# Kernel tuning notes

Measured on AMD Instinct MI355X. Metric: run time of the kernel, lower is better.

## Reference

```python
import jax, jax.numpy as jnp
import numpy as np
from jax import lax

RANK = 4
N_ITERS = 20  # fixed ALS iteration count (tensorly default caps at 100 with tol; fixed count for jit)
EPS = 1e-6


def _khatri_rao(U, V):
    # column-wise Kronecker: (m, r) x (n, r) -> (m*n, r), row index i*n + j
    r = U.shape[1]
    return (U[:, None, :] * V[None, :, :]).reshape(-1, r)


def _cp_als_mode0(T, A, B, C):
    # CP-ALS on 3-way tensor T [I,J,K]; returns mode-0 factor A [I, r]
    I, J, K = T.shape
    T0 = T.reshape(I, J * K)                       # cols indexed j*K+k
    T1 = jnp.moveaxis(T, 1, 0).reshape(J, I * K)   # cols indexed i*K+k
    T2 = jnp.moveaxis(T, 2, 0).reshape(K, I * J)   # cols indexed i*J+j
    eye = EPS * jnp.eye(RANK, dtype=T.dtype)

    def step(carry, _):
        A, B, C = carry
        G = (B.T @ B) * (C.T @ C) + eye
        A = jnp.linalg.solve(G, (T0 @ _khatri_rao(B, C)).T).T
        G = (A.T @ A) * (C.T @ C) + eye
        B = jnp.linalg.solve(G, (T1 @ _khatri_rao(A, C)).T).T
        G = (A.T @ A) * (B.T @ B) + eye
        C = jnp.linalg.solve(G, (T2 @ _khatri_rao(A, B)).T).T
        return (A, B, C), None

    (A, B, C), _ = lax.scan(step, (A, B, C), None, length=N_ITERS)
    return A


def setup_inputs() -> dict:
    key = jax.random.key(0)
    ks = jax.random.split(key, 8)
    b, c, h, w = 256, 512, 14, 14
    red = 16
    x = jax.random.uniform(ks[0], (b, c, h, w), dtype=jnp.float32)
    # random ALS init factors (per sample)
    A0 = jax.random.uniform(ks[1], (b, c, RANK), dtype=jnp.float32)
    B0 = jax.random.uniform(ks[2], (b, h, RANK), dtype=jnp.float32)
    C0 = jax.random.uniform(ks[3], (b, w, RANK), dtype=jnp.float32)
    # rank_fc: Linear(rank,rank,bias=False), Linear(rank,1,bias=False)
    w1 = jax.random.normal(ks[4], (RANK, RANK), dtype=jnp.float32) / np.sqrt(RANK)
    w2 = jax.random.normal(ks[5], (1, RANK), dtype=jnp.float32) / np.sqrt(RANK)
    # fc: Linear(c, c//red), Linear(c//red, c)
    fw1 = jax.random.normal(ks[6], (c // red, c), dtype=jnp.float32) / np.sqrt(c)
    fw2 = jax.random.normal(ks[7], (c, c // red), dtype=jnp.float32) / np.sqrt(c // red)
    return {"x": x, "A0": A0, "B0": B0, "C0": C0, "w1": w1, "w2": w2, "fw1": fw1, "fw2": fw2}


def reference(x, A0, B0, C0, w1, w2, fw1, fw2):
    b, c, _, _ = x.shape
    # per-sample CP decomposition; keep channel-mode factor [b, c, rank]
    A = jax.vmap(_cp_als_mode0)(x, A0, B0, C0)
    # rank_fc: (b,c,rank) -> (b,c)
    y = jnp.maximum(jnp.einsum('bcr,sr->bcs', A, w1), 0.0)
    y = jnp.einsum('bcs,os->bco', y, w2)[..., 0]
    # SE fc: (b,c) -> sigmoid gate
    y = jnp.maximum(y @ fw1.T, 0.0)
    y = jax.nn.sigmoid(y @ fw2.T)
    return x * y[:, :, None, None]
```

## Files before the change

kernel.cpp:

```cpp
#include <hip/hip_runtime.h>


#define EPSV 1e-6f

#define SM_ATA  104

typedef __attribute__((ext_vector_type(8))) short short8;
typedef __attribute__((ext_vector_type(4))) float float4v;

struct SMem {
  union {
    struct {
      short xhi[4 * 13 * 64 * 8];
      short xlo[4 * 13 * 64 * 8];
    } p1;
    struct {
      union {
        float gram[196 * 197];
        struct {
          short fh[7 * 64 * 8];
          short fl[7 * 64 * 8];
          float part[512 * 5];
        } f;
      } g;
      float H[196 * 5];
      float Y[196 * 5];
    } p2;
  } u;
  float B[56];
  float C[56];
  float Sm[120];
};

__device__ __forceinline__ float rlane(float v, int l) {
  return __uint_as_float(__builtin_amdgcn_readlane(__float_as_uint(v), l));
}
__device__ __forceinline__ void fence_lds() { __threadfence_block(); }

__device__ __forceinline__ unsigned bf16rne(float f) {
  unsigned u = __float_as_uint(f);
  return (u + 0x7FFFu + ((u >> 16) & 1u)) >> 16;
}

__device__ __forceinline__ float gram16(const float* V, int l) {
  int r = (l >> 2) & 3, s = l & 3;
  float a = 0.f;
#pragma unroll
  for (int j = 0; j < 14; ++j) a += V[j * 4 + r] * V[j * 4 + s];
  return a;
}

__device__ __forceinline__ float sel4(float a, float b, float c, float d, int k) {
  float x = (k & 1) ? b : a;
  float y = (k & 1) ? d : c;
  return (k & 2) ? y : x;
}

__device__ __forceinline__ void ginv_lanes(float myG, float gv[16]) {
  const float a00 = rlane(myG, 0),  a01 = rlane(myG, 1),  a02 = rlane(myG, 2),  a03 = rlane(myG, 3);
  const float a10 = rlane(myG, 4),  a11 = rlane(myG, 5),  a12 = rlane(myG, 6),  a13 = rlane(myG, 7);
  const float a20 = rlane(myG, 8),  a21 = rlane(myG, 9),  a22 = rlane(myG, 10), a23 = rlane(myG, 11);
  const float a30 = rlane(myG, 12), a31 = rlane(myG, 13), a32 = rlane(myG, 14), a33 = rlane(myG, 15);
  const float s0 = a00*a11 - a10*a01, s1 = a00*a12 - a10*a02, s2 = a00*a13 - a10*a03;
  const float s3 = a01*a12 - a11*a02, s4 = a01*a13 - a11*a03, s5 = a02*a13 - a12*a03;
  const float c5 = a22*a33 - a32*a23, c4 = a21*a33 - a31*a23, c3 = a21*a32 - a31*a22;
  const float c2 = a20*a33 - a30*a23, c1 = a20*a32 - a30*a22, c0 = a20*a31 - a30*a21;
  const float det = s0*c5 - s1*c4 + s2*c3 + s3*c2 - s4*c1 + s5*c0;
  const float rd = 1.0f / det;
  gv[0]  = ( a11*c5 - a12*c4 + a13*c3) * rd;
  gv[1]  = (-a01*c5 + a02*c4 - a03*c3) * rd;
  gv[2]  = ( a31*s5 - a32*s4 + a33*s3) * rd;
  gv[3]  = (-a21*s5 + a22*s4 - a23*s3) * rd;
  gv[4]  = (-a10*c5 + a12*c2 - a13*c1) * rd;
  gv[5]  = ( a00*c5 - a02*c2 + a03*c1) * rd;
  gv[6]  = (-a30*s5 + a32*s2 - a33*s1) * rd;
  gv[7]  = ( a20*s5 - a22*s2 + a23*s1) * rd;
  gv[8]  = ( a10*c4 - a11*c2 + a13*c0) * rd;
  gv[9]  = (-a00*c4 + a01*c2 - a03*c0) * rd;
  gv[10] = ( a30*s4 - a31*s2 + a33*s0) * rd;
  gv[11] = (-a20*s4 + a21*s2 - a23*s0) * rd;
  gv[12] = (-a10*c3 + a11*c1 - a12*c0) * rd;
  gv[13] = ( a00*c3 - a01*c1 + a02*c0) * rd;
  gv[14] = (-a30*s3 + a31*s1 - a32*s0) * rd;
  gv[15] = ( a20*s3 - a21*s1 + a22*s0) * rd;
}

__device__ __forceinline__ void computeH_scatter(SMem* sm, int l, const float gv[16]) {
#pragma unroll
  for (int k4 = 0; k4 < 4; ++k4) {
    int p = l + 64 * k4;
    if (p < 196) {
      int j = p / 14, kk = p - j * 14;
      float kr[4];
#pragma unroll
      for (int s = 0; s < 4; ++s) kr[s] = sm->B[j * 4 + s] * sm->C[kk * 4 + s];
      int kb = p >> 5, ii = p & 7, lrow = ((p >> 3) & 3) * 16;
#pragma unroll
      for (int r = 0; r < 4; ++r) {
        float h = kr[0] * gv[0 + r] + kr[1] * gv[4 + r]
                + kr[2] * gv[8 + r] + kr[3] * gv[12 + r];
        sm->u.p2.H[p * 5 + r] = h;
        unsigned hh = bf16rne(h);
        float hf = __uint_as_float(hh << 16);
        unsigned ll = bf16rne(h - hf);
        int fi = (kb * 64 + lrow + r) * 8 + ii;
        sm->u.p2.g.f.fh[fi] = (short)hh;
        sm->u.p2.g.f.fl[fi] = (short)ll;
      }
    }
  }
}

__device__ __forceinline__ void initial_H(SMem* sm, int l) {
  float btb = gram16(sm->B, l);
  float ctc = gram16(sm->C, l);
  float dgl = ((l >> 2) == (l & 3)) ? EPSV : 0.f;
  float myG = btb * ctc + dgl;
  float gv[16];
  ginv_lanes(myG, gv);
  computeH_scatter(sm, l, gv);
}

__device__ __forceinline__ void factor_update(SMem* sm, int l) {
  const int jj = l >> 2, r = l & 3;
  const float dgl = ((l >> 2) == (l & 3)) ? EPSV : 0.f;
  float gv[16];
  float btb_new;
  {
    float ctc_old = gram16(sm->C, l);
    float ata = sm->Sm[SM_ATA + (l & 15)];
    ginv_lanes(ata * ctc_old + dgl, gv);
    float m = 0.f;
    if (l < 56) {
#pragma unroll
      for (int k = 0; k < 14; ++k) m += sm->u.p2.Y[(jj * 14 + k) * 5 + r] * sm->C[k * 4 + r];
    }
    float bn = 0.f;
#pragma unroll
    for (int e = 0; e < 4; ++e) {
      float me = e ? __shfl_xor(m, e, 64) : m;
      float coef = sel4(gv[((0 ^ e) << 2) + 0], gv[((1 ^ e) << 2) + 1],
                        gv[((2 ^ e) << 2) + 2], gv[((3 ^ e) << 2) + 3], r);
      bn += me * coef;
    }
    if (l < 56) sm->B[l] = bn;
  }
  fence_lds();
  {
    btb_new = gram16(sm->B, l);
    float ata = sm->Sm[SM_ATA + (l & 15)];
    ginv_lanes(ata * btb_new + dgl, gv);
    float m = 0.f;
    if (l < 56) {
#pragma unroll
      for (int j = 0; j < 14; ++j) m += sm->u.p2.Y[(j * 14 + jj) * 5 + r] * sm->B[j * 4 + r];
    }
    float cn = 0.f;
#pragma unroll
    for (int e = 0; e < 4; ++e) {
      float me = e ? __shfl_xor(m, e, 64) : m;
      float coef = sel4(gv[((0 ^ e) << 2) + 0], gv[((1 ^ e) << 2) + 1],
                        gv[((2 ^ e) << 2) + 2], gv[((3 ^ e) << 2) + 3], r);
      cn += me * coef;
    }
    if (l < 56) sm->C[l] = cn;
  }
  fence_lds();
  {
    float ctc_new = gram16(sm->C, l);
    ginv_lanes(btb_new * ctc_new + dgl, gv);
    computeH_scatter(sm, l, gv);
  }
}

extern "C" __global__ void __launch_bounds__(1024, 4)
dese_kernel(const float* __restrict__ x, const float* __restrict__ B0,
            const float* __restrict__ C0, const float* __restrict__ w1,
            const float* __restrict__ w2, const float* __restrict__ fw1,
            const float* __restrict__ fw2, float* __restrict__ out) {
  extern __shared__ char smraw[];
  SMem* sm = (SMem*)smraw;
  const int tid = threadIdx.x;
  const int b = blockIdx.x;
  const int wv = tid >> 6;
  const int lane = tid & 63;
  const float* xb = x + (size_t)b * 100352;

  if (tid < 56) sm->B[tid] = B0[b * 56 + tid];
  if (tid >= 64 && tid < 120) sm->C[tid - 64] = C0[b * 56 + (tid - 64)];

  {
    const int R = (wv >= 4) + (wv >= 7) + (wv >= 10) + (wv >= 12) + (wv >= 14) + (wv >= 15);
    const int base = (R == 0) ? 0 : (R == 1) ? 4 : (R == 2) ? 7 : (R == 3) ? 10
                   : (R == 4) ? 12 : (R == 5) ? 14 : 15;
    const int I0 = 2 * R;
    const int J0 = I0 + 4 * (wv - base);
    const int IC1 = (I0 + 1 <= 12) ? I0 + 1 : 12;
    const bool iok1 = (I0 + 1 <= 12);

    float4v acc0[4], acc1[4];
#pragma unroll
    for (int i = 0; i < 4; ++i) {
      acc0[i] = (float4v){0.f, 0.f, 0.f, 0.f};
      acc1[i] = (float4v){0.f, 0.f, 0.f, 0.f};
    }

    for (int chunk = 0; chunk < 4; ++chunk) {
      __syncthreads();
#pragma unroll
      for (int t = 0; t < 4; ++t) {
        int u = wv + 16 * t;
        if (u < 52) {
          int s = u / 13, pt = u - s * 13;
          int p = pt * 16 + (lane & 15);
          int chb = chunk * 128 + s * 32 + (lane >> 4) * 8;
          unsigned hp[4], lp[4];
#pragma unroll
          for (int ii = 0; ii < 8; ++ii) {
            float v = 0.f;
            if (p < 196) v = xb[(size_t)(chb + ii) * 196 + p];
            unsigned h = bf16rne(v);
            float hf = __uint_as_float(h << 16);
            unsigned lo2 = bf16rne(v - hf);
            if (ii & 1) { hp[ii >> 1] |= (h << 16); lp[ii >> 1] |= (lo2 << 16); }
            else        { hp[ii >> 1] = h;          lp[ii >> 1] = lo2; }
          }
          int fidx = (s * 13 + pt) * 64 + lane;
          *(uint4*)&sm->u.p1.xhi[fidx * 8] = make_uint4(hp[0], hp[1], hp[2], hp[3]);
          *(uint4*)&sm->u.p1.xlo[fidx * 8] = make_uint4(lp[0], lp[1], lp[2], lp[3]);
        }
      }
      __syncthreads();
#pragma unroll
      for (int s = 0; s < 4; ++s) {
        const short8 aH0 = *(const short8*)&sm->u.p1.xhi[((s * 13 + I0)  * 64 + lane) * 8];
        const short8 aL0 = *(const short8*)&sm->u.p1.xlo[((s * 13 + I0)  * 64 + lane) * 8];
        const short8 aH1 = *(const short8*)&sm->u.p1.xhi[((s * 13 + IC1) * 64 + lane) * 8];
        const short8 aL1 = *(const short8*)&sm->u.p1.xlo[((s * 13 + IC1) * 64 + lane) * 8];
#pragma unroll
        for (int j = 0; j < 4; ++j) {
          const int J = J0 + j;
          if (J <= 12) {
            const short8 bH = *(const short8*)&sm->u.p1.xhi[((s * 13 + J) * 64 + lane) * 8];
            const short8 bL = *(const short8*)&sm->u.p1.xlo[((s * 13 + J) * 64 + lane) * 8];
            acc0[j] = __builtin_amdgcn_mfma_f32_16x16x32_bf16(aH0, bH, acc0[j], 0, 0, 0);
            acc0[j] = __builtin_amdgcn_mfma_f32_16x16x32_bf16(aH0, bL, acc0[j], 0, 0, 0);
            acc0[j] = __builtin_amdgcn_mfma_f32_16x16x32_bf16(aL0, bH, acc0[j], 0, 0, 0);
            if (iok1 && I0 + 1 <= J) {
              acc1[j] = __builtin_amdgcn_mfma_f32_16x16x32_bf16(aH1, bH, acc1[j], 0, 0, 0);
              acc1[j] = __builtin_amdgcn_mfma_f32_16x16x32_bf16(aH1, bL, acc1[j], 0, 0, 0);
              acc1[j] = __builtin_amdgcn_mfma_f32_16x16x32_bf16(aL1, bH, acc1[j], 0, 0, 0);
            }
          }
        }
      }
    }
    __syncthreads();
    {
      int col = lane & 15, quad = lane >> 4;
#define WRITE_TILE(ACC, I)                                          \
      {                                                             \
        int pc = (J0 + j) * 16 + col;                               \
        _Pragma("unroll")                                           \
        for (int reg = 0; reg < 4; ++reg) {                         \
          int pr = (I) * 16 + quad * 4 + reg;                       \
          if (pr < 196 && pc < 196) {                               \
            float v = ACC[j][reg];                                  \
            sm->u.p2.g.gram[pr * 197 + pc] = v;                     \
            sm->u.p2.g.gram[pc * 197 + pr] = v;                     \
          }                                                         \
        }                                                           \
      }
#pragma unroll
      for (int j = 0; j < 4; ++j) {
        const int J = J0 + j;
        if (J <= 12) {
          WRITE_TILE(acc0, I0)
          if (iok1 && I0 + 1 <= J) WRITE_TILE(acc1, I0 + 1)
        }
      }
#undef WRITE_TILE
    }
  }
  __syncthreads();

  short8 afh[7], afl[7];
  if (wv < 13) {
    const int m = wv * 16 + (lane & 15);
    const int mok = (m < 196);
    const int kq = (lane >> 4) * 8;
#pragma unroll
    for (int kb = 0; kb < 7; ++kb) {
#pragma unroll
      for (int i = 0; i < 8; ++i) {
        int k = kb * 32 + kq + i;
        float v = (mok && k < 196) ? sm->u.p2.g.gram[m * 197 + k] : 0.f;
        unsigned h = bf16rne(v);
        float hf = __uint_as_float(h << 16);
        unsigned lo = bf16rne(v - hf);
        afh[kb][i] = (short)h;
        afl[kb][i] = (short)lo;
      }
    }
  }
  __syncthreads();
  {
    unsigned* z = (unsigned*)sm->u.p2.g.f.fh;
#pragma unroll
    for (int t = 0; t < 4; ++t) {
      int idx = tid + 1024 * t;
      if (idx < 3584) z[idx] = 0u;
    }
  }
  __syncthreads();

  if (tid < 64) initial_H(sm, lane);
  __syncthreads();

  for (int it = 0; it < 19; ++it) {
    if (wv < 13) {
      float4v ac0 = {0.f, 0.f, 0.f, 0.f}, ac1 = {0.f, 0.f, 0.f, 0.f};
#pragma unroll
      for (int kb = 0; kb < 7; ++kb) {
        const short8 bh = *(const short8*)&sm->u.p2.g.f.fh[(kb * 64 + lane) * 8];
        const short8 bl = *(const short8*)&sm->u.p2.g.f.fl[(kb * 64 + lane) * 8];
        if (kb & 1) {
          ac1 = __builtin_amdgcn_mfma_f32_16x16x32_bf16(afh[kb], bh, ac1, 0, 0, 0);
          ac1 = __builtin_amdgcn_mfma_f32_16x16x32_bf16(afh[kb], bl, ac1, 0, 0, 0);
          ac1 = __builtin_amdgcn_mfma_f32_16x16x32_bf16(afl[kb], bh, ac1, 0, 0, 0);
        } else {
          ac0 = __builtin_amdgcn_mfma_f32_16x16x32_bf16(afh[kb], bh, ac0, 0, 0, 0);
          ac0 = __builtin_amdgcn_mfma_f32_16x16x32_bf16(afh[kb], bl, ac0, 0, 0, 0);
          ac0 = __builtin_amdgcn_mfma_f32_16x16x32_bf16(afl[kb], bh, ac0, 0, 0, 0);
        }
      }
      float4v acc = ac0 + ac1;
      int col = lane & 15;
      int row0 = wv * 16 + ((lane >> 4) << 2);
      if (col < 4) {
#pragma unroll
        for (int reg = 0; reg < 4; ++reg) {
          int pr = row0 + reg;
          if (pr < 196) sm->u.p2.Y[pr * 5 + col] = acc[reg];
        }
      }
    }
    __syncthreads();
    {
      int r = wv >> 2, s = wv & 3;
      float a = 0.f;
#pragma unroll
      for (int k4 = 0; k4 < 4; ++k4) {
        int p = lane + 64 * k4;
        if (p < 196) a += sm->u.p2.H[p * 5 + r] * sm->u.p2.Y[p * 5 + s];
      }
#pragma unroll
      for (int m = 32; m > 0; m >>= 1) a += __shfl_xor(a, m, 64);
      if (lane == 0) sm->Sm[SM_ATA + wv] = a;
    }
    __syncthreads();
    if (tid < 64) factor_update(sm, lane);
    __syncthreads();
  }

  {
    float hr[13];
#pragma unroll
    for (int k = 0; k < 13; ++k) {
      int d = 64 * k + lane;
      hr[k] = (d < 784) ? sm->u.p2.H[(d >> 2) * 5 + (d & 3)] : 0.f;
    }
    const int ch = tid & 511;
    const int half = tid >> 9;
    const float4* row = (const float4*)(xb + ch * 196);
    float a0 = 0.f, a1 = 0.f, a2 = 0.f, a3 = 0.f;
#define EPI_F4(F4)                                                     \
    {                                                                  \
      float4 v = row[(F4)];                                            \
      float vv[4] = {v.x, v.y, v.z, v.w};                              \
      _Pragma("unroll")                                                \
      for (int j = 0; j < 4; ++j) {                                    \
        int d = 16 * (F4) + 4 * j;                                     \
        a0 += vv[j] * rlane(hr[(d + 0) >> 6], (d + 0) & 63);           \
        a1 += vv[j] * rlane(hr[(d + 1) >> 6], (d + 1) & 63);           \
        a2 += vv[j] * rlane(hr[(d + 2) >> 6], (d + 2) & 63);           \
        a3 += vv[j] * rlane(hr[(d + 3) >> 6], (d + 3) & 63);           \
      }                                                                \
    }
    if (half == 0) {
#pragma unroll
      for (int f4 = 0; f4 < 25; ++f4) EPI_F4(f4)
    } else {
#pragma unroll
      for (int f4 = 25; f4 < 49; ++f4) EPI_F4(f4)
    }
#undef EPI_F4
    if (half) {
      float* pp = &sm->u.p2.g.f.part[ch * 5];
      pp[0] = a0; pp[1] = a1; pp[2] = a2; pp[3] = a3;
    }
    __syncthreads();
    if (tid < 512) {
      const float* pp = &sm->u.p2.g.f.part[tid * 5];
      a0 += pp[0]; a1 += pp[1]; a2 += pp[2]; a3 += pp[3];
      float y = 0.f;
#pragma unroll
      for (int s = 0; s < 4; ++s) {
        float pre = w1[s * 4 + 0] * a0 + w1[s * 4 + 1] * a1 + w1[s * 4 + 2] * a2
                  + w1[s * 4 + 3] * a3;
        y += w2[s] * fmaxf(pre, 0.f);
      }
      sm->u.p2.Y[tid] = y;
    }
  }
  __syncthreads();
  {
    int u = tid >> 5, lc = tid & 31;
    float a = 0.f;
#pragma unroll
    for (int k = 0; k < 16; ++k) {
      int c = lc + 32 * k;
      a += sm->u.p2.Y[c] * fw1[u * 512 + c];
    }
    a += __shfl_xor(a, 1, 64);
    a += __shfl_xor(a, 2, 64);
    a += __shfl_xor(a, 4, 64);
    a += __shfl_xor(a, 8, 64);
    a += __shfl_xor(a, 16, 64);
    if (lc == 0) sm->u.p2.Y[512 + u] = fmaxf(a, 0.f);
  }
  __syncthreads();
  if (tid < 512) {
    const float4* f2r = (const float4*)(fw2 + tid * 32);
    float za = 0.f;
#pragma unroll
    for (int u4 = 0; u4 < 8; ++u4) {
      float4 fv = f2r[u4];
      za += fv.x * sm->u.p2.Y[512 + u4 * 4 + 0];
      za += fv.y * sm->u.p2.Y[512 + u4 * 4 + 1];
      za += fv.z * sm->u.p2.Y[512 + u4 * 4 + 2];
      za += fv.w * sm->u.p2.Y[512 + u4 * 4 + 3];
    }
    float g = 1.f / (1.f + __expf(-za));
    sm->u.p2.Y[tid] = g;
  }
  __syncthreads();
  {
    const float4* xi = (const float4*)xb;
    float4* oo = (float4*)(out + (size_t)b * 100352);
#pragma unroll
    for (int t = 0; t < 25; ++t) {
      int v = tid + t * 1024;
      if (v < 25088) {
        float4 q = xi[v];
        float g = sm->u.p2.Y[v / 49];
        oo[v] = make_float4(q.x * g, q.y * g, q.z * g, q.w * g);
      }
    }
  }
}

extern "C" void kernel_launch(void* const* d_in, const int* in_sizes, int n_in,
                              void* d_out, int out_size, void* d_ws, size_t ws_size,
                              hipStream_t stream) {
  (void)in_sizes; (void)n_in; (void)d_ws; (void)ws_size; (void)out_size;
  const float* x   = (const float*)d_in[0];
  const float* B0  = (const float*)d_in[2];
  const float* C0  = (const float*)d_in[3];
  const float* w1  = (const float*)d_in[4];
  const float* w2  = (const float*)d_in[5];
  const float* fw1 = (const float*)d_in[6];
  const float* fw2 = (const float*)d_in[7];
  float* out = (float*)d_out;

  size_t shmem = sizeof(SMem);
  hipFuncSetAttribute((const void*)dese_kernel,
                      hipFuncAttributeMaxDynamicSharedMemorySize, (int)shmem);
  hipLaunchKernelGGL(dese_kernel, dim3(256), dim3(1024), shmem, stream,
                     x, B0, C0, w1, w2, fw1, fw2, out);
}
```

Before: 370.3 us.

## Prefetch x chunks into registers, fuse ATA reduction into MFMA epilogue, skip last scatter

The Gram-building phase now loads the next chunk of x into registers right after the LDS barrier, so the global loads overlap with the MFMA work on the current chunk. In the ALS loop, the H^T·Y reduction is computed inside the Y-producing waves using shuffles and LDS atomics, which removes one full block barrier per iteration. A spare wave computes C^T C in parallel. The bf16 scatter of H is skipped on the final iteration. In exchange it adds register pressure from the prefetch buffer, and LDS atomics make the float summation order nondeterministic.

New measurement: 364.3 us. About the same (-1.6%).

```diff
diff --git a/kernel.cpp b/kernel.cpp
--- a/kernel.cpp
+++ b/kernel.cpp
@@ -3,6 +3,7 @@
 
 #define EPSV 1e-6f
 
+#define SM_CTC  32
 #define SM_ATA  104
 
 typedef __attribute__((ext_vector_type(8))) short short8;
@@ -85,7 +86,8 @@
   gv[15] = ( a20*s3 - a21*s1 + a22*s0) * rd;
 }
 
-__device__ __forceinline__ void computeH_scatter(SMem* sm, int l, const float gv[16]) {
+__device__ __forceinline__ void computeH_scatter(SMem* sm, int l, const float gv[16],
+                                                 bool scatter) {
 #pragma unroll
   for (int k4 = 0; k4 < 4; ++k4) {
     int p = l + 64 * k4;
@@ -100,12 +102,14 @@
         float h = kr[0] * gv[0 + r] + kr[1] * gv[4 + r]
                 + kr[2] * gv[8 + r] + kr[3] * gv[12 + r];
         sm->u.p2.H[p * 5 + r] = h;
-        unsigned hh = bf16rne(h);
-        float hf = __uint_as_float(hh << 16);
-        unsigned ll = bf16rne(h - hf);
-        int fi = (kb * 64 + lrow + r) * 8 + ii;
-        sm->u.p2.g.f.fh[fi] = (short)hh;
-        sm->u.p2.g.f.fl[fi] = (short)ll;
+        if (scatter) {
+          unsigned hh = bf16rne(h);
+          float hf = __uint_as_float(hh << 16);
+          unsigned ll = bf16rne(h - hf);
+          int fi = (kb * 64 + lrow + r) * 8 + ii;
+          sm->u.p2.g.f.fh[fi] = (short)hh;
+          sm->u.p2.g.f.fl[fi] = (short)ll;
+        }
       }
     }
   }
@@ -118,17 +122,19 @@
   float myG = btb * ctc + dgl;
   float gv[16];
   ginv_lanes(myG, gv);
-  computeH_scatter(sm, l, gv);
-}
-
-__device__ __forceinline__ void factor_update(SMem* sm, int l) {
+  if (l < 16) sm->Sm[SM_ATA + l] = 0.f;
+  computeH_scatter(sm, l, gv, true);
+}
+
+__device__ __forceinline__ void factor_update(SMem* sm, int l, bool last) {
   const int jj = l >> 2, r = l & 3;
   const float dgl = ((l >> 2) == (l & 3)) ? EPSV : 0.f;
+  const float ata = sm->Sm[SM_ATA + (l & 15)];
+  const float ctc_old = sm->Sm[SM_CTC + (l & 15)];
+  if (l < 16) sm->Sm[SM_ATA + l] = 0.f;
   float gv[16];
   float btb_new;
   {
-    float ctc_old = gram16(sm->C, l);
-    float ata = sm->Sm[SM_ATA + (l & 15)];
     ginv_lanes(ata * ctc_old + dgl, gv);
     float m = 0.f;
     if (l < 56) {
@@ -148,7 +154,6 @@
   fence_lds();
   {
     btb_new = gram16(sm->B, l);
-    float ata = sm->Sm[SM_ATA + (l & 15)];
     ginv_lanes(ata * btb_new + dgl, gv);
     float m = 0.f;
     if (l < 56) {
@@ -169,7 +174,7 @@
   {
     float ctc_new = gram16(sm->C, l);
     ginv_lanes(btb_new * ctc_new + dgl, gv);
-    computeH_scatter(sm, l, gv);
+    computeH_scatter(sm, l, gv, !last);
   }
 }
 
@@ -198,6 +203,34 @@
     const int IC1 = (I0 + 1 <= 12) ? I0 + 1 : 12;
     const bool iok1 = (I0 + 1 <= 12);
 
+    int us_[4], upt_[4];
+    bool uv_[4];
+#pragma unroll
+    for (int t = 0; t < 4; ++t) {
+      int u = wv + 16 * t;
+      uv_[t] = (u < 52);
+      int s = uv_[t] ? (u / 13) : 0;
+      us_[t] = s;
+      upt_[t] = uv_[t] ? (u - s * 13) : 0;
+    }
+    const int pp_ = (lane & 15);
+    const int co_ = (lane >> 4) * 8;
+
+    float xr[4][8];
+#define ISSUE_LOADS(CHUNK)                                                    \
+    {                                                                         \
+      _Pragma("unroll")                                                       \
+      for (int t = 0; t < 4; ++t) {                                           \
+        if (uv_[t]) {                                                         \
+          int p = upt_[t] * 16 + pp_;                                         \
+          int chb = (CHUNK) * 128 + us_[t] * 32 + co_;                        \
+          _Pragma("unroll")                                                   \
+          for (int ii = 0; ii < 8; ++ii)                                      \
+            xr[t][ii] = (p < 196) ? xb[(size_t)(chb + ii) * 196 + p] : 0.f;   \
+        }                                                                     \
+      }                                                                       \
+    }
+
     float4v acc0[4], acc1[4];
 #pragma unroll
     for (int i = 0; i < 4; ++i) {
@@ -205,32 +238,29 @@
       acc1[i] = (float4v){0.f, 0.f, 0.f, 0.f};
     }
 
+    ISSUE_LOADS(0)
     for (int chunk = 0; chunk < 4; ++chunk) {
       __syncthreads();
 #pragma unroll
       for (int t = 0; t < 4; ++t) {
-        int u = wv + 16 * t;
-        if (u < 52) {
-          int s = u / 13, pt = u - s * 13;
-          int p = pt * 16 + (lane & 15);
-          int chb = chunk * 128 + s * 32 + (lane >> 4) * 8;
+        if (uv_[t]) {
           unsigned hp[4], lp[4];
 #pragma unroll
           for (int ii = 0; ii < 8; ++ii) {
-            float v = 0.f;
-            if (p < 196) v = xb[(size_t)(chb + ii) * 196 + p];
+            float v = xr[t][ii];
             unsigned h = bf16rne(v);
             float hf = __uint_as_float(h << 16);
             unsigned lo2 = bf16rne(v - hf);
             if (ii & 1) { hp[ii >> 1] |= (h << 16); lp[ii >> 1] |= (lo2 << 16); }
             else        { hp[ii >> 1] = h;          lp[ii >> 1] = lo2; }
           }
-          int fidx = (s * 13 + pt) * 64 + lane;
+          int fidx = (us_[t] * 13 + upt_[t]) * 64 + lane;
           *(uint4*)&sm->u.p1.xhi[fidx * 8] = make_uint4(hp[0], hp[1], hp[2], hp[3]);
           *(uint4*)&sm->u.p1.xlo[fidx * 8] = make_uint4(lp[0], lp[1], lp[2], lp[3]);
         }
       }
       __syncthreads();
+      if (chunk < 3) ISSUE_LOADS(chunk + 1)
 #pragma unroll
       for (int s = 0; s < 4; ++s) {
         const short8 aH0 = *(const short8*)&sm->u.p1.xhi[((s * 13 + I0)  * 64 + lane) * 8];
@@ -255,6 +285,7 @@
         }
       }
     }
+#undef ISSUE_LOADS
     __syncthreads();
     {
       int col = lane & 15, quad = lane >> 4;
@@ -335,31 +366,44 @@
         }
       }
       float4v acc = ac0 + ac1;
-      int col = lane & 15;
-      int row0 = wv * 16 + ((lane >> 4) << 2);
+      const int col = lane & 15;
+      const int quad = lane >> 4;
+      const int row0 = wv * 16 + quad * 4;
       if (col < 4) {
 #pragma unroll
         for (int reg = 0; reg < 4; ++reg) {
           int pr = row0 + reg;
           if (pr < 196) sm->u.p2.Y[pr * 5 + col] = acc[reg];
         }
-      }
+        float pa0 = 0.f, pa1 = 0.f, pa2 = 0.f, pa3 = 0.f;
+#pragma unroll
+        for (int reg = 0; reg < 4; ++reg) {
+          int pr = row0 + reg;
+          if (pr < 196) {
+            float yv = acc[reg];
+            pa0 += sm->u.p2.H[pr * 5 + 0] * yv;
+            pa1 += sm->u.p2.H[pr * 5 + 1] * yv;
+            pa2 += sm->u.p2.H[pr * 5 + 2] * yv;
+            pa3 += sm->u.p2.H[pr * 5 + 3] * yv;
+          }
+        }
+        pa0 += __shfl_xor(pa0, 16, 64); pa0 += __shfl_xor(pa0, 32, 64);
+        pa1 += __shfl_xor(pa1, 16, 64); pa1 += __shfl_xor(pa1, 32, 64);
+        pa2 += __shfl_xor(pa2, 16, 64); pa2 += __shfl_xor(pa2, 32, 64);
+        pa3 += __shfl_xor(pa3, 16, 64); pa3 += __shfl_xor(pa3, 32, 64);
+        if (quad == 0) {
+          atomicAdd(&sm->Sm[SM_ATA + 0 * 4 + col], pa0);
+          atomicAdd(&sm->Sm[SM_ATA + 1 * 4 + col], pa1);
+          atomicAdd(&sm->Sm[SM_ATA + 2 * 4 + col], pa2);
+          atomicAdd(&sm->Sm[SM_ATA + 3 * 4 + col], pa3);
+        }
+      }
+    } else if (wv == 13) {
+      float ctc = gram16(sm->C, lane);
+      if (lane < 16) sm->Sm[SM_CTC + lane] = ctc;
     }
     __syncthreads();
-    {
-      int r = wv >> 2, s = wv & 3;
-      float a = 0.f;
-#pragma unroll
-      for (int k4 = 0; k4 < 4; ++k4) {
-        int p = lane + 64 * k4;
-        if (p < 196) a += sm->u.p2.H[p * 5 + r] * sm->u.p2.Y[p * 5 + s];
-      }
-#pragma unroll
-      for (int m = 32; m > 0; m >>= 1) a += __shfl_xor(a, m, 64);
-      if (lane == 0) sm->Sm[SM_ATA + wv] = a;
-    }
-    __syncthreads();
-    if (tid < 64) factor_update(sm, lane);
+    if (tid < 64) factor_update(sm, lane, it == 18);
     __syncthreads();
   }
 
```
